# Kernel tuning notes

Measured on AMD Instinct MI355X. Metric: run time of the kernel, lower is better.

## Reference

```python
import jax, jax.numpy as jnp
import numpy as np

B, H, C, D = 32, 12, 512, 768
M = 8            # mentions per entity
EMB, BLK = 768, 8
NCLS, NER = 97, 6
OFFSET = 1       # [CLS] offset as in get_hrt


def setup_inputs() -> dict:
    key = jax.random.key(0)
    ks = jax.random.split(key, 10)
    sequence_output = jax.random.normal(ks[0], (B, C, D), jnp.float32)
    attention = jax.random.uniform(ks[1], (B, H, C, C), jnp.float32)
    ner_tags = jax.random.uniform(ks[2], (B, 2, NER), jnp.float32)
    W_head = jax.random.normal(ks[3], (EMB, 2 * D + NER), jnp.float32) * 0.02
    b_head = jnp.zeros((EMB,), jnp.float32)
    W_tail = jax.random.normal(ks[4], (EMB, 2 * D + NER), jnp.float32) * 0.02
    b_tail = jnp.zeros((EMB,), jnp.float32)
    W_bil = jax.random.normal(ks[5], (NCLS, EMB * BLK), jnp.float32) * 0.02
    b_bil = jnp.zeros((NCLS,), jnp.float32)
    entity_pos = jax.random.randint(ks[6], (B, 2, M), 0, C - 2)
    return {"sequence_output": sequence_output, "attention": attention,
            "ner_tags": ner_tags, "W_head": W_head, "b_head": b_head,
            "W_tail": W_tail, "b_tail": b_tail, "W_bil": W_bil,
            "b_bil": b_bil, "entity_pos": entity_pos}


def reference(sequence_output, attention, ner_tags, W_head, b_head,
              W_tail, b_tail, W_bil, b_bil, entity_pos):
    # --- get_hrt, fully vectorized over batch/entities/mentions ---
    pos = entity_pos + OFFSET                       # [B,2,M], all < C
    bidx = jnp.arange(B)[:, None, None]             # [B,1,1]
    # mention embeddings gather + logsumexp over mentions
    ment_emb = sequence_output[bidx, pos]           # [B,2,M,D]
    ent_emb = jax.scipy.special.logsumexp(ment_emb, axis=2)  # [B,2,D]
    # mention attention-row gather + mean over mentions
    att_t = attention.transpose(0, 2, 1, 3)         # [B,C,H,C]
    ment_att = att_t[bidx, pos]                     # [B,2,M,H,C]
    ent_att = ment_att.mean(axis=2)                 # [B,2,H,C]
    # head/tail = entities 0 and 1
    hs = ent_emb[:, 0]                              # [B,D]
    ht_att = (ent_att[:, 0] * ent_att[:, 1]).mean(axis=1)    # [B,C] (mean over heads)
    ht_att = ht_att / (ht_att.sum(axis=1, keepdims=True) + 1e-5)
    rs = jnp.einsum('bld,bl->bd', sequence_output, ht_att)   # [B,D]
    # --- extractors (note: original code concatenates hs in BOTH inputs) ---
    hs_inp = jnp.concatenate([hs, rs, ner_tags[:, 0]], axis=1)  # [B,2D+NER]
    ts_inp = jnp.concatenate([hs, rs, ner_tags[:, 1]], axis=1)  # faithful to source
    hs_f = jnp.tanh(hs_inp @ W_head.T + b_head)     # [B,EMB]
    ts_f = jnp.tanh(ts_inp @ W_tail.T + b_tail)     # [B,EMB]
    # --- grouped bilinear block ---
    b1 = hs_f.reshape(B, EMB // BLK, BLK)
    b2 = ts_f.reshape(B, EMB // BLK, BLK)
    bl = (b1[:, :, :, None] * b2[:, :, None, :]).reshape(B, EMB * BLK)
    logits = bl @ W_bil.T + b_bil                   # [B,NCLS]
    return logits
```

## Files before the change

### kernel.cpp

```cpp
#include <hip/hip_runtime.h>
#include <math.h>

#define BB 32
#define HH 12
#define CC 512
#define DD 768
#define MM 8
#define NER 6
#define NCLS 97
#define KTOT 1542
#define OFFS 1
#define KCH 193


__global__ void k_att(const float* __restrict__ att, const int* __restrict__ epos,
                      float* __restrict__ rawp) {
    int b = blockIdx.x, h = blockIdx.y;
    __shared__ int pos[16];
    if (threadIdx.x < 16) pos[threadIdx.x] = epos[b * 16 + threadIdx.x] + OFFS;
    __syncthreads();
    int c = threadIdx.x;
    const float* base = att + ((size_t)(b * HH + h)) * CC * CC;
    float a0 = 0.f, a1 = 0.f;
#pragma unroll
    for (int m = 0; m < MM; m++) {
        a0 += base[(size_t)pos[m] * CC + c];
        a1 += base[(size_t)pos[MM + m] * CC + c];
    }
    rawp[((size_t)(b * HH + h)) * CC + c] = a0 * a1 * (1.0f / (MM * MM * HH));
}

__global__ void k_rs_part(const float* __restrict__ seq, const float* __restrict__ rawp,
                          float* __restrict__ rs_part, float* __restrict__ Sb) {
    int b = blockIdx.x, cc = blockIdx.y, t = threadIdx.x;
    __shared__ float wsm[32];
    if (t < 32) {
        float s = 0.f;
#pragma unroll
        for (int h = 0; h < HH; h++)
            s += rawp[((size_t)(b * HH + h)) * CC + cc * 32 + t];
        wsm[t] = s;
    }
    __syncthreads();
    float4 acc = {0.f, 0.f, 0.f, 0.f};
    const float* sp = seq + ((size_t)b * CC + cc * 32) * DD + t * 4;
#pragma unroll 4
    for (int ci = 0; ci < 32; ci++) {
        float w = wsm[ci];
        float4 v = *(const float4*)(sp + (size_t)ci * DD);
        acc.x += v.x * w; acc.y += v.y * w; acc.z += v.z * w; acc.w += v.w * w;
    }
    *(float4*)&rs_part[((size_t)(b * 16 + cc)) * DD + t * 4] = acc;
    if (cc == 0) {
        __shared__ float sb[192];
        float s = 0.f;
        const float* rp = rawp + (size_t)b * HH * CC;
        for (int i = t; i < HH * CC; i += 192) s += rp[i];
        sb[t] = s;
        __syncthreads();
        if (t == 0) {
            float tot = 0.f;
            for (int i = 0; i < 192; i++) tot += sb[i];
            Sb[b] = tot;
        }
    }
}

__global__ void k_rs_hs(const float* __restrict__ seq, const int* __restrict__ epos,
                        const float* __restrict__ rs_part, const float* __restrict__ Sb,
                        float* __restrict__ rs, float* __restrict__ hs) {
    int b = blockIdx.x, t = threadIdx.x;
    __shared__ int pos[MM];
    if (t < MM) pos[t] = epos[b * 16 + t] + OFFS;
    __syncthreads();
    float4 acc = {0.f, 0.f, 0.f, 0.f};
    for (int cc = 0; cc < 16; cc++) {
        float4 p = *(const float4*)&rs_part[((size_t)(b * 16 + cc)) * DD + t * 4];
        acc.x += p.x; acc.y += p.y; acc.z += p.z; acc.w += p.w;
    }
    float inv = 1.0f / (Sb[b] + 1e-5f);
    float4 r = {acc.x * inv, acc.y * inv, acc.z * inv, acc.w * inv};
    *(float4*)&rs[b * DD + t * 4] = r;

    float xs0[MM], xs1[MM], xs2[MM], xs3[MM];
#pragma unroll
    for (int m = 0; m < MM; m++) {
        float4 v = *(const float4*)&seq[((size_t)b * CC + pos[m]) * DD + t * 4];
        xs0[m] = v.x; xs1[m] = v.y; xs2[m] = v.z; xs3[m] = v.w;
    }
    float o[4];
    float* xs[4] = {xs0, xs1, xs2, xs3};
#pragma unroll
    for (int comp = 0; comp < 4; comp++) {
        float mx = xs[comp][0];
#pragma unroll
        for (int m = 1; m < MM; m++) mx = fmaxf(mx, xs[comp][m]);
        float se = 0.f;
#pragma unroll
        for (int m = 0; m < MM; m++) se += expf(xs[comp][m] - mx);
        o[comp] = logf(se) + mx;
    }
    float4 hv = {o[0], o[1], o[2], o[3]};
    *(float4*)&hs[b * DD + t * 4] = hv;
}

__global__ void k_headtail(const float* __restrict__ hs, const float* __restrict__ rs,
                           const float* __restrict__ ner, const float* __restrict__ Wh,
                           const float* __restrict__ Wt, float* __restrict__ accp) {
    int kt = blockIdx.x, jt = blockIdx.y, e = blockIdx.z;
    int kstart = kt * KCH;
    int klen = min(KCH, KTOT - kstart);
    __shared__ float A[32][KCH];
    for (int i = threadIdx.x; i < 32 * KCH; i += 256) {
        int bb = i / KCH, kk = i - bb * KCH;
        int k = kstart + kk;
        float v = 0.f;
        if (k < KTOT) {
            if (k < DD) v = hs[bb * DD + k];
            else if (k < 2 * DD) v = rs[bb * DD + (k - DD)];
            else v = ner[(bb * 2 + e) * NER + (k - 2 * DD)];
        }
        A[bb][kk] = v;
    }
    __syncthreads();
    int b = threadIdx.x & 31, jq = threadIdx.x >> 5;
    int j0 = jt * 64 + jq * 8;
    const float* W = e ? Wt : Wh;
    const float* Wb = W + (size_t)j0 * KTOT + kstart;
    float acc[8] = {0.f, 0.f, 0.f, 0.f, 0.f, 0.f, 0.f, 0.f};
#pragma unroll 4
    for (int kk = 0; kk < klen; kk++) {
        float a = A[b][kk];
#pragma unroll
        for (int jj = 0; jj < 8; jj++) acc[jj] += a * Wb[(size_t)jj * KTOT + kk];
    }
    float* outp = accp + (((size_t)(kt * 2 + e)) * BB + b) * DD + j0;
#pragma unroll
    for (int jj = 0; jj < 8; jj++) outp[jj] = acc[jj];
}

__global__ void k_tanh(const float* __restrict__ accp, const float* __restrict__ bh,
                       const float* __restrict__ bt, float* __restrict__ fbuf) {
    int x = blockIdx.x * 256 + threadIdx.x;
    int e = x / (BB * DD);
    int r = x - e * (BB * DD);
    int j = r % DD;
    float s = e ? bt[j] : bh[j];
#pragma unroll
    for (int kt = 0; kt < 8; kt++) s += accp[(size_t)kt * (2 * BB * DD) + x];
    fbuf[x] = tanhf(s);
}

__global__ void k_bil(const float* __restrict__ fbuf, const float* __restrict__ Wb,
                      const float* __restrict__ bbil, float* __restrict__ out) {
    int n = blockIdx.x;
    int g = threadIdx.x & 7, b = threadIdx.x >> 3;
    const float* hsf = fbuf + b * DD;
    const float* tsf = fbuf + (32 + b) * DD;
    const float* W = Wb + (size_t)n * (DD * 8);
    float acc = 0.f;
    for (int t = 0; t < 12; t++) {
        int f = g + 8 * t;
        float4 h0 = *(const float4*)&hsf[f * 8];
        float4 h1 = *(const float4*)&hsf[f * 8 + 4];
        float4 t0 = *(const float4*)&tsf[f * 8];
        float4 t1 = *(const float4*)&tsf[f * 8 + 4];
        float hv[8] = {h0.x, h0.y, h0.z, h0.w, h1.x, h1.y, h1.z, h1.w};
        float tv[8] = {t0.x, t0.y, t0.z, t0.w, t1.x, t1.y, t1.z, t1.w};
        const float* wf = W + f * 64;
#pragma unroll
        for (int i = 0; i < 8; i++) {
            float4 w0 = *(const float4*)&wf[i * 8];
            float4 w1 = *(const float4*)&wf[i * 8 + 4];
            float dot = tv[0] * w0.x + tv[1] * w0.y + tv[2] * w0.z + tv[3] * w0.w
                      + tv[4] * w1.x + tv[5] * w1.y + tv[6] * w1.z + tv[7] * w1.w;
            acc += hv[i] * dot;
        }
    }
    __shared__ float part[32 * 9];
    part[b * 9 + g] = acc;
    __syncthreads();
    if (g == 0) {
        float s = 0.f;
#pragma unroll
        for (int i = 0; i < 8; i++) s += part[b * 9 + i];
        out[b * NCLS + n] = s + bbil[n];
    }
}

extern "C" void kernel_launch(void* const* d_in, const int* in_sizes, int n_in,
                              void* d_out, int out_size, void* d_ws, size_t ws_size,
                              hipStream_t stream) {
    const float* seq  = (const float*)d_in[0];
    const float* att  = (const float*)d_in[1];
    const float* ner  = (const float*)d_in[2];
    const float* Wh   = (const float*)d_in[3];
    const float* bh   = (const float*)d_in[4];
    const float* Wt   = (const float*)d_in[5];
    const float* bt   = (const float*)d_in[6];
    const float* Wbil = (const float*)d_in[7];
    const float* bbil = (const float*)d_in[8];
    const int*   epos = (const int*)d_in[9];
    float* out = (float*)d_out;
    float* ws = (float*)d_ws;

    float* rawp    = ws;
    float* Sb      = ws + 196608;
    float* rs_part = ws + 196640;
    float* rs      = ws + 589856;
    float* hs      = ws + 614432;
    float* accp    = ws + 639008;
    float* fbuf    = ws + 1032224;

    k_att<<<dim3(BB, HH), 512, 0, stream>>>(att, epos, rawp);
    k_rs_part<<<dim3(BB, 16), 192, 0, stream>>>(seq, rawp, rs_part, Sb);
    k_rs_hs<<<BB, 192, 0, stream>>>(seq, epos, rs_part, Sb, rs, hs);
    k_headtail<<<dim3(8, 12, 2), 256, 0, stream>>>(hs, rs, ner, Wh, Wt, accp);
    k_tanh<<<192, 256, 0, stream>>>(accp, bh, bt, fbuf);
    k_bil<<<NCLS, 256, 0, stream>>>(fbuf, Wbil, bbil, out);
}
```

Before: 566.7 us.

## Fuse attention gather into rs partials and fold hs/rs assembly into headtail

The attention-row gather is merged into the rs partial kernel, so rawp is no longer written and re-read. Each block computes its own 32-column weight slice and a per-chunk sum. The k_rs_hs kernel is removed: logsumexp over mentions and the reduction of rs partials now happen inside k_headtail's shared-memory fill, which cuts two launches and the intermediate buffers. The cost is that hs/rs work is repeated across the 24 (jt,e) blocks of headtail. The bilinear kernel also moves to 512 threads with 16 groups per batch row.

```diff
diff --git a/kernel.cpp b/kernel.cpp
--- a/kernel.cpp
+++ b/kernel.cpp
@@ -13,35 +13,48 @@
 #define KCH 193
 
 
-__global__ void k_att(const float* __restrict__ att, const int* __restrict__ epos,
-                      float* __restrict__ rawp) {
-    int b = blockIdx.x, h = blockIdx.y;
-    __shared__ int pos[16];
-    if (threadIdx.x < 16) pos[threadIdx.x] = epos[b * 16 + threadIdx.x] + OFFS;
-    __syncthreads();
-    int c = threadIdx.x;
-    const float* base = att + ((size_t)(b * HH + h)) * CC * CC;
-    float a0 = 0.f, a1 = 0.f;
-#pragma unroll
-    for (int m = 0; m < MM; m++) {
-        a0 += base[(size_t)pos[m] * CC + c];
-        a1 += base[(size_t)pos[MM + m] * CC + c];
-    }
-    rawp[((size_t)(b * HH + h)) * CC + c] = a0 * a1 * (1.0f / (MM * MM * HH));
-}
-
-__global__ void k_rs_part(const float* __restrict__ seq, const float* __restrict__ rawp,
-                          float* __restrict__ rs_part, float* __restrict__ Sb) {
+__global__ void k_rs_att(const float* __restrict__ seq, const float* __restrict__ att,
+                         const int* __restrict__ epos, float* __restrict__ rs_part,
+                         float* __restrict__ Sbp) {
     int b = blockIdx.x, cc = blockIdx.y, t = threadIdx.x;
+    __shared__ int pos16[16];
+    __shared__ float part[6][32];
     __shared__ float wsm[32];
+    if (t < 16) pos16[t] = epos[b * 16 + t] + OFFS;
+    __syncthreads();
+
+    {
+        int c = t & 31, hg = t >> 5;
+        int cglob = cc * 32 + c;
+        float p = 0.f;
+        for (int hh = 0; hh < 2; hh++) {
+            int h = hg + 6 * hh;
+            const float* base = att + ((size_t)(b * HH + h)) * CC * CC + cglob;
+            float a0 = 0.f, a1 = 0.f;
+#pragma unroll
+            for (int m = 0; m < MM; m++) {
+                a0 += base[(size_t)pos16[m] * CC];
+                a1 += base[(size_t)pos16[MM + m] * CC];
+            }
+            p += a0 * a1;
+        }
+        part[hg][c] = p;
+    }
+    __syncthreads();
     if (t < 32) {
+        float w = 0.f;
+#pragma unroll
+        for (int hg = 0; hg < 6; hg++) w += part[hg][t];
+        wsm[t] = w * (1.0f / (MM * MM * HH));
+    }
+    __syncthreads();
+    if (t == 0) {
         float s = 0.f;
 #pragma unroll
-        for (int h = 0; h < HH; h++)
-            s += rawp[((size_t)(b * HH + h)) * CC + cc * 32 + t];
-        wsm[t] = s;
-    }
-    __syncthreads();
+        for (int c = 0; c < 32; c++) s += wsm[c];
+        Sbp[b * 16 + cc] = s;
+    }
+
     float4 acc = {0.f, 0.f, 0.f, 0.f};
     const float* sp = seq + ((size_t)b * CC + cc * 32) * DD + t * 4;
 #pragma unroll 4
@@ -51,79 +64,61 @@
         acc.x += v.x * w; acc.y += v.y * w; acc.z += v.z * w; acc.w += v.w * w;
     }
     *(float4*)&rs_part[((size_t)(b * 16 + cc)) * DD + t * 4] = acc;
-    if (cc == 0) {
-        __shared__ float sb[192];
-        float s = 0.f;
-        const float* rp = rawp + (size_t)b * HH * CC;
-        for (int i = t; i < HH * CC; i += 192) s += rp[i];
-        sb[t] = s;
-        __syncthreads();
-        if (t == 0) {
-            float tot = 0.f;
-            for (int i = 0; i < 192; i++) tot += sb[i];
-            Sb[b] = tot;
-        }
-    }
-}
-
-__global__ void k_rs_hs(const float* __restrict__ seq, const int* __restrict__ epos,
-                        const float* __restrict__ rs_part, const float* __restrict__ Sb,
-                        float* __restrict__ rs, float* __restrict__ hs) {
-    int b = blockIdx.x, t = threadIdx.x;
-    __shared__ int pos[MM];
-    if (t < MM) pos[t] = epos[b * 16 + t] + OFFS;
-    __syncthreads();
-    float4 acc = {0.f, 0.f, 0.f, 0.f};
-    for (int cc = 0; cc < 16; cc++) {
-        float4 p = *(const float4*)&rs_part[((size_t)(b * 16 + cc)) * DD + t * 4];
-        acc.x += p.x; acc.y += p.y; acc.z += p.z; acc.w += p.w;
-    }
-    float inv = 1.0f / (Sb[b] + 1e-5f);
-    float4 r = {acc.x * inv, acc.y * inv, acc.z * inv, acc.w * inv};
-    *(float4*)&rs[b * DD + t * 4] = r;
-
-    float xs0[MM], xs1[MM], xs2[MM], xs3[MM];
-#pragma unroll
-    for (int m = 0; m < MM; m++) {
-        float4 v = *(const float4*)&seq[((size_t)b * CC + pos[m]) * DD + t * 4];
-        xs0[m] = v.x; xs1[m] = v.y; xs2[m] = v.z; xs3[m] = v.w;
-    }
-    float o[4];
-    float* xs[4] = {xs0, xs1, xs2, xs3};
-#pragma unroll
-    for (int comp = 0; comp < 4; comp++) {
-        float mx = xs[comp][0];
-#pragma unroll
-        for (int m = 1; m < MM; m++) mx = fmaxf(mx, xs[comp][m]);
-        float se = 0.f;
-#pragma unroll
-        for (int m = 0; m < MM; m++) se += expf(xs[comp][m] - mx);
-        o[comp] = logf(se) + mx;
-    }
-    float4 hv = {o[0], o[1], o[2], o[3]};
-    *(float4*)&hs[b * DD + t * 4] = hv;
-}
-
-__global__ void k_headtail(const float* __restrict__ hs, const float* __restrict__ rs,
-                           const float* __restrict__ ner, const float* __restrict__ Wh,
+}
+
+__global__ void k_headtail(const float* __restrict__ seq, const float* __restrict__ rs_part,
+                           const float* __restrict__ Sbp, const float* __restrict__ ner,
+                           const int* __restrict__ epos, const float* __restrict__ Wh,
                            const float* __restrict__ Wt, float* __restrict__ accp) {
     int kt = blockIdx.x, jt = blockIdx.y, e = blockIdx.z;
     int kstart = kt * KCH;
     int klen = min(KCH, KTOT - kstart);
     __shared__ float A[32][KCH];
-    for (int i = threadIdx.x; i < 32 * KCH; i += 256) {
+    __shared__ int poss[32][MM];
+    __shared__ float invS[32];
+    int tid = threadIdx.x;
+    if (tid < 256) {
+        int bb = tid >> 3, m = tid & 7;
+        poss[bb][m] = epos[bb * 16 + m] + OFFS;
+    }
+    if (tid < 32) {
+        float s = 0.f;
+#pragma unroll
+        for (int c = 0; c < 16; c++) s += Sbp[tid * 16 + c];
+        invS[tid] = 1.0f / (s + 1e-5f);
+    }
+    __syncthreads();
+
+    for (int i = tid; i < 32 * KCH; i += 256) {
         int bb = i / KCH, kk = i - bb * KCH;
         int k = kstart + kk;
         float v = 0.f;
-        if (k < KTOT) {
-            if (k < DD) v = hs[bb * DD + k];
-            else if (k < 2 * DD) v = rs[bb * DD + (k - DD)];
-            else v = ner[(bb * 2 + e) * NER + (k - 2 * DD)];
+        if (k < DD) {
+            const float* srow = seq + (size_t)bb * CC * DD + k;
+            float x[MM];
+#pragma unroll
+            for (int m = 0; m < MM; m++) x[m] = srow[(size_t)poss[bb][m] * DD];
+            float mx = x[0];
+#pragma unroll
+            for (int m = 1; m < MM; m++) mx = fmaxf(mx, x[m]);
+            float se = 0.f;
+#pragma unroll
+            for (int m = 0; m < MM; m++) se += expf(x[m] - mx);
+            v = logf(se) + mx;
+        } else if (k < 2 * DD) {
+            int d = k - DD;
+            float s = 0.f;
+#pragma unroll
+            for (int c = 0; c < 16; c++) s += rs_part[((size_t)(bb * 16 + c)) * DD + d];
+            v = s * invS[bb];
+        } else if (k < KTOT) {
+            v = ner[(bb * 2 + e) * NER + (k - 2 * DD)];
         }
         A[bb][kk] = v;
     }
     __syncthreads();
-    int b = threadIdx.x & 31, jq = threadIdx.x >> 5;
+
+    int b = tid & 31, jq = tid >> 5;
     int j0 = jt * 64 + jq * 8;
     const float* W = e ? Wt : Wh;
     const float* Wb = W + (size_t)j0 * KTOT + kstart;
@@ -154,13 +149,13 @@
 __global__ void k_bil(const float* __restrict__ fbuf, const float* __restrict__ Wb,
                       const float* __restrict__ bbil, float* __restrict__ out) {
     int n = blockIdx.x;
-    int g = threadIdx.x & 7, b = threadIdx.x >> 3;
+    int g = threadIdx.x & 15, b = threadIdx.x >> 4;
     const float* hsf = fbuf + b * DD;
     const float* tsf = fbuf + (32 + b) * DD;
     const float* W = Wb + (size_t)n * (DD * 8);
     float acc = 0.f;
-    for (int t = 0; t < 12; t++) {
-        int f = g + 8 * t;
+    for (int t = 0; t < 6; t++) {
+        int f = g + 16 * t;
         float4 h0 = *(const float4*)&hsf[f * 8];
         float4 h1 = *(const float4*)&hsf[f * 8 + 4];
         float4 t0 = *(const float4*)&tsf[f * 8];
@@ -177,13 +172,13 @@
             acc += hv[i] * dot;
         }
     }
-    __shared__ float part[32 * 9];
-    part[b * 9 + g] = acc;
+    __shared__ float part[32 * 17];
+    part[b * 17 + g] = acc;
     __syncthreads();
     if (g == 0) {
         float s = 0.f;
 #pragma unroll
-        for (int i = 0; i < 8; i++) s += part[b * 9 + i];
+        for (int i = 0; i < 16; i++) s += part[b * 17 + i];
         out[b * NCLS + n] = s + bbil[n];
     }
 }
@@ -204,18 +199,13 @@
     float* out = (float*)d_out;
     float* ws = (float*)d_ws;
 
-    float* rawp    = ws;
-    float* Sb      = ws + 196608;
-    float* rs_part = ws + 196640;
-    float* rs      = ws + 589856;
-    float* hs      = ws + 614432;
-    float* accp    = ws + 639008;
-    float* fbuf    = ws + 1032224;
-
-    k_att<<<dim3(BB, HH), 512, 0, stream>>>(att, epos, rawp);
-    k_rs_part<<<dim3(BB, 16), 192, 0, stream>>>(seq, rawp, rs_part, Sb);
-    k_rs_hs<<<BB, 192, 0, stream>>>(seq, epos, rs_part, Sb, rs, hs);
-    k_headtail<<<dim3(8, 12, 2), 256, 0, stream>>>(hs, rs, ner, Wh, Wt, accp);
+    float* Sbp     = ws;
+    float* rs_part = ws + 512;
+    float* accp    = ws + 393728;
+    float* fbuf    = ws + 786944;
+
+    k_rs_att<<<dim3(BB, 16), 192, 0, stream>>>(seq, att, epos, rs_part, Sbp);
+    k_headtail<<<dim3(8, 12, 2), 256, 0, stream>>>(seq, rs_part, Sbp, ner, epos, Wh, Wt, accp);
     k_tanh<<<192, 256, 0, stream>>>(accp, bh, bt, fbuf);
-    k_bil<<<NCLS, 256, 0, stream>>>(fbuf, Wbil, bbil, out);
-}
+    k_bil<<<NCLS, 512, 0, stream>>>(fbuf, Wbil, bbil, out);
+}
```

New measurement: 559.9 us. About the same (-1.2%).
